# Performance work log

Measured on AMD Instinct MI355X. Metric: run time of the kernel, lower is better.

Reference implementation:

```python
import jax, jax.numpy as jnp
import numpy as np

B, N, D, H = 2, 2048, 1024, 16
DH = D // H  # 64


def setup_inputs() -> dict:
    key = jax.random.key(0)
    ks = jax.random.split(key, 5)
    s = 1.0 / np.sqrt(D)
    x = jax.random.normal(ks[0], (B, N, D), jnp.float32)
    # per-head kqv Linear weights, stacked: [H, D, 3*DH]
    Wkqv = jax.random.normal(ks[1], (H, D, 3 * DH), jnp.float32) * s
    bkqv = jax.random.normal(ks[2], (H, 3 * DH), jnp.float32) * 0.02
    Wo = jax.random.normal(ks[3], (D, D), jnp.float32) * s
    bo = jax.random.normal(ks[4], (D,), jnp.float32) * 0.02
    return {"x": x, "Wkqv": Wkqv, "bkqv": bkqv, "Wo": Wo, "bo": bo}


def reference(x, Wkqv, bkqv, Wo, bo):
    Bs, Ns, Ds = x.shape
    Hs = Wkqv.shape[0]
    dh = Wkqv.shape[-1] // 3
    # all heads' kqv projections at once: [B, H, N, 3*dh]
    kqv_out = jnp.einsum('bnd,hde->bhne', x, Wkqv) + bkqv[None, :, None, :]
    # original splits in order (k, q, v)
    k, q, v = jnp.split(kqv_out, 3, axis=-1)
    # NOTE: original computes attention_scores(k, q) = k @ q^T (swapped vs standard)
    A = jnp.einsum('bhnd,bhmd->bhnm', k, q) / jnp.sqrt(jnp.asarray(dh, x.dtype))
    mask = jnp.tril(jnp.ones((Ns, Ns), dtype=bool))
    A = jnp.where(mask[None, None], A, -jnp.inf)
    alpha = jax.nn.softmax(A, axis=-1)
    sa = jnp.einsum('bhnm,bhmd->bhnd', alpha, v)  # [B, H, N, dh]
    # concat heads along feature dim (head0..headH-1 order)
    sa = sa.transpose(0, 2, 1, 3).reshape(Bs, Ns, Hs * dh)
    return sa @ Wo + bo
```

## Files before the change

kernel.cpp:

```cpp
#include <hip/hip_runtime.h>
#include <hip/hip_bf16.h>
#include <cstdint>
#include <cstddef>

typedef __bf16 bf16x8 __attribute__((ext_vector_type(8)));
typedef __bf16 bf16x4 __attribute__((ext_vector_type(4)));
typedef float  f32x4  __attribute__((ext_vector_type(4)));

constexpr int Bc = 2, Nc = 2048, Dc = 1024, Hc = 16, DHc = 64;
constexpr int BN = Bc * Nc;
constexpr int E3 = 3 * DHc;
constexpr int BH = Bc * Hc;
constexpr int NK = Hc * E3;

__device__ __forceinline__ f32x4 mfma16(bf16x8 a, bf16x8 b, f32x4 c) {
  return __builtin_amdgcn_mfma_f32_16x16x32_bf16(a, b, c, 0, 0, 0);
}

__device__ __forceinline__ void gload16(const __bf16* g, __bf16* l) {
  __builtin_amdgcn_global_load_lds((const __attribute__((address_space(1))) void*)g,
                                   (__attribute__((address_space(3))) void*)l,
                                   16, 0, 0);
}

__global__ void cvt_x_kernel(const float* __restrict__ x, __bf16* __restrict__ xb) {
  int i = (blockIdx.x * 256 + threadIdx.x) * 4;
  float4 v = *(const float4*)(x + i);
  xb[i + 0] = (__bf16)v.x;
  xb[i + 1] = (__bf16)v.y;
  xb[i + 2] = (__bf16)v.z;
  xb[i + 3] = (__bf16)v.w;
}

constexpr int TP = 68;
__global__ void cvt_T_kernel(const float* __restrict__ src, __bf16* __restrict__ dst,
                             int R, int C) {
  __shared__ __bf16 T[64][TP];
  const int c0 = blockIdx.x * 64, r0 = blockIdx.y * 64;
  const size_t sbase = (size_t)blockIdx.z * R * C;
  const int tid = threadIdx.x;
#pragma unroll
  for (int it = 0; it < 4; ++it) {
    int g = tid + it * 256;
    int r = g >> 4, c4 = (g & 15) * 4;
    float4 v = *(const float4*)&src[sbase + (size_t)(r0 + r) * C + c0 + c4];
    T[c4 + 0][r] = (__bf16)v.x;
    T[c4 + 1][r] = (__bf16)v.y;
    T[c4 + 2][r] = (__bf16)v.z;
    T[c4 + 3][r] = (__bf16)v.w;
  }
  __syncthreads();
#pragma unroll
  for (int it = 0; it < 2; ++it) {
    int g = tid + it * 256;
    int c = g >> 3, ch = (g & 7) * 8;
    bf16x4 u0 = *(const bf16x4*)&T[c][ch];
    bf16x4 u1 = *(const bf16x4*)&T[c][ch + 4];
    __bf16* dp = &dst[sbase + (size_t)(c0 + c) * R + r0 + ch];
    *(bf16x4*)dp = u0;
    *(bf16x4*)(dp + 4) = u1;
  }
}

__launch_bounds__(256)
__global__ void kqv_gemm_kernel(const __bf16* __restrict__ xb,
                                const __bf16* __restrict__ wkt,
                                const float* __restrict__ bkqv,
                                __bf16* __restrict__ kqv,
                                __bf16* __restrict__ vT) {
  const int mt = blockIdx.x;
  const int nt = blockIdx.y;
  __shared__ __align__(16) __bf16 Al[2][128][64];
  __shared__ __align__(16) __bf16 Bl[2][128][64];
  const int tid  = threadIdx.x;
  const int lane = tid & 63;
  const int w    = tid >> 6;
  const int fr   = lane & 15, fq = lane >> 4;
  const int fq4  = fq * 4;
  const int WR   = (w >> 1) * 64, WC = (w & 1) * 64;
  const int sr   = tid >> 3;
  const int sc8  = ((tid & 7) ^ (sr & 7)) * 8;
  const int wb   = (w << 3);
  const int m0   = mt * 128, n0 = nt * 128;

  auto STAGE = [&](int buf, int k0) {
#pragma unroll
    for (int j = 0; j < 4; ++j)
      gload16(&xb[(size_t)(m0 + j * 32 + sr) * Dc + k0 + sc8], &Al[buf][j * 32 + wb][0]);
#pragma unroll
    for (int j = 0; j < 4; ++j)
      gload16(&wkt[(size_t)(n0 + j * 32 + sr) * Dc + k0 + sc8], &Bl[buf][j * 32 + wb][0]);
  };

  f32x4 acc[4][4] = {};
  STAGE(0, 0);
  int cur = 0;
  for (int t = 0; t < 16; ++t) {
    if (t < 15) {
      STAGE(cur ^ 1, (t + 1) * 64);
      asm volatile("s_waitcnt vmcnt(8)" ::: "memory");
    } else {
      asm volatile("s_waitcnt vmcnt(0)" ::: "memory");
    }
    asm volatile("s_barrier" ::: "memory");
    const char* Ab = (const char*)&Al[cur][0][0];
    const char* Bb = (const char*)&Bl[cur][0][0];
#pragma unroll
    for (int ks = 0; ks < 2; ++ks) {
      bf16x8 a_[4], b_[4];
#pragma unroll
      for (int mr = 0; mr < 4; ++mr) {
        int r = WR + mr * 16 + fr;
        a_[mr] = *(const bf16x8*)(Ab + r * 128 + ((ks * 64 + fq * 16) ^ ((r & 7) << 4)));
      }
#pragma unroll
      for (int nc = 0; nc < 4; ++nc) {
        int r = WC + nc * 16 + fr;
        b_[nc] = *(const bf16x8*)(Bb + r * 128 + ((ks * 64 + fq * 16) ^ ((r & 7) << 4)));
      }
#pragma unroll
      for (int mr = 0; mr < 4; ++mr)
#pragma unroll
        for (int nc = 0; nc < 4; ++nc)
          acc[mr][nc] = mfma16(a_[mr], b_[nc], acc[mr][nc]);
    }
    asm volatile("s_barrier" ::: "memory");
    cur ^= 1;
  }

  const int b = m0 >> 11;
#pragma unroll
  for (int nc = 0; nc < 4; ++nc) {
    const int nb = n0 + WC + nc * 16;
    const int h  = nb / 192;
    const int eb = nb - h * 192;
    const float bias = bkqv[nb + fr];
    if (eb < 64) {
      const float sc = 0.125f * 1.44269504088896f;
      const int el = eb + fr;
#pragma unroll
      for (int mr = 0; mr < 4; ++mr) {
        int nn0 = (m0 & (Nc - 1)) + WR + mr * 16 + fq4;
        bf16x4 v4;
#pragma unroll
        for (int i = 0; i < 4; ++i) v4[i] = (__bf16)((acc[mr][nc][i] + bias) * sc);
        *(bf16x4*)&kqv[((size_t)((b * Hc + h) * DHc + el)) * Nc + nn0] = v4;
      }
    } else if (eb < 128) {
      const int e = (eb - 64) + fr;
      __bf16* dst = kqv + (size_t)BH * Nc * DHc +
                    ((size_t)(b * Hc + h)) * Nc * DHc + e;
#pragma unroll
      for (int mr = 0; mr < 4; ++mr)
#pragma unroll
        for (int i = 0; i < 4; ++i) {
          int n = (m0 & (Nc - 1)) + WR + mr * 16 + fq4 + i;
          dst[(size_t)n * DHc] = (__bf16)(acc[mr][nc][i] + bias);
        }
    } else {
      const int el = eb - 128 + fr;
#pragma unroll
      for (int mr = 0; mr < 4; ++mr) {
        int nn0 = (m0 & (Nc - 1)) + WR + mr * 16 + fq4;
        bf16x4 v4;
#pragma unroll
        for (int i = 0; i < 4; ++i) v4[i] = (__bf16)(acc[mr][nc][i] + bias);
        *(bf16x4*)&vT[((size_t)((b * Hc + h) * DHc + el)) * Nc + nn0] = v4;
      }
    }
  }
}

__launch_bounds__(256)
__global__ void attn_kernel(const __bf16* __restrict__ kT,
                            const __bf16* __restrict__ qb,
                            const __bf16* __restrict__ vT,
                            __bf16* __restrict__ sab) {
  const int bx = blockIdx.x;
  const int by = blockIdx.y;
  const int bh   = 4 * (bx & 7) + (by >> 3);
  const int pair = (bx >> 3) * 8 + (by & 7);
  __shared__ __align__(16) __bf16 KqL[2][64][64];
  __shared__ __align__(16) __bf16 VtL[2][64][64];
  __shared__ __align__(16) __bf16 Pl[4][16][64];
  const int tid  = threadIdx.x;
  const int lane = tid & 63;
  const int w    = tid >> 6;
  const int fr   = lane & 15, fq = lane >> 4;
  const int fq4  = fq * 4;
  const int key  = (fr & 7) << 4;
  const int off0 = (fq * 16) ^ key;
  const int off1 = (fq * 16 + 64) ^ key;
  const __bf16* kth = kT + (size_t)bh * DHc * Nc;
  const __bf16* qbh = qb + (size_t)bh * Nc * DHc;
  const __bf16* vth = vT + (size_t)bh * DHc * Nc;
  const int b = bh >> 4, h = bh & 15;
  char* Pw = (char*)&Pl[w][0][0];

  const int sch  = (tid & 7);
  const int r_s0 = tid >> 3;
  const int r_s1 = r_s0 + 32;
  const int swb0 = r_s0 * 128 + ((sch * 16) ^ ((r_s0 & 7) << 4));
  const int swb1 = r_s1 * 128 + ((sch * 16) ^ ((r_s1 & 7) << 4));

  for (int ph = 0; ph < 2; ++ph) {
    const int qt   = ph ? (31 - pair) : pair;
    const int n0   = qt * 64 + w * 16;
    const int ncol = n0 + fr;

    bf16x8 bq0, bq1;
#pragma unroll
    for (int j = 0; j < 8; ++j) {
      bq0[j] = kth[(size_t)(8 * fq + j) * Nc + n0 + fr];
      bq1[j] = kth[(size_t)(32 + 8 * fq + j) * Nc + n0 + fr];
    }

    float l_run = 0.f;
    f32x4 acc[4] = {};

    __syncthreads();
    {
      bf16x8 k0a = *(const bf16x8*)&qbh[(size_t)r_s0 * DHc + sch * 8];
      bf16x8 k0b = *(const bf16x8*)&qbh[(size_t)r_s1 * DHc + sch * 8];
      bf16x8 v0a = *(const bf16x8*)&vth[(size_t)r_s0 * Nc + sch * 8];
      bf16x8 v0b = *(const bf16x8*)&vth[(size_t)r_s1 * Nc + sch * 8];
      *(bf16x8*)((char*)&KqL[0][0][0] + swb0) = k0a;
      *(bf16x8*)((char*)&KqL[0][0][0] + swb1) = k0b;
      *(bf16x8*)((char*)&VtL[0][0][0] + swb0) = v0a;
      *(bf16x8*)((char*)&VtL[0][0][0] + swb1) = v0b;
    }
    __syncthreads();

    int cur = 0;
    for (int t = 0; t <= qt; ++t) {
      bf16x8 nk0, nk1, nv0, nv1;
      const bool more = (t < qt);
      if (more) {
        const int v1 = (t + 1) * 64;
        nk0 = *(const bf16x8*)&qbh[(size_t)(v1 + r_s0) * DHc + sch * 8];
        nk1 = *(const bf16x8*)&qbh[(size_t)(v1 + r_s1) * DHc + sch * 8];
        nv0 = *(const bf16x8*)&vth[(size_t)r_s0 * Nc + v1 + sch * 8];
        nv1 = *(const bf16x8*)&vth[(size_t)r_s1 * Nc + v1 + sch * 8];
      }

      const char* Kqb = (const char*)&KqL[cur][0][0];
      const char* Vtb = (const char*)&VtL[cur][0][0];

      f32x4 s[4];
      __builtin_amdgcn_s_setprio(1);
#pragma unroll
      for (int c = 0; c < 4; ++c) {
        const char* rp = Kqb + (c * 16 + fr) * 128;
        bf16x8 t0 = *(const bf16x8*)(rp + off0);
        bf16x8 t1 = *(const bf16x8*)(rp + off1);
        f32x4 z = {};
        z = mfma16(t0, bq0, z);
        z = mfma16(t1, bq1, z);
        s[c] = z;
      }
      __builtin_amdgcn_s_setprio(0);

      if (t == qt) {
        const int thr = ncol - t * 64;
#pragma unroll
        for (int c = 0; c < 4; ++c)
#pragma unroll
          for (int i = 0; i < 4; ++i) {
            float pv = exp2f(s[c][i]);
            s[c][i] = (c * 16 + fq4 + i > thr) ? 0.f : pv;
          }
      } else {
#pragma unroll
        for (int c = 0; c < 4; ++c)
#pragma unroll
          for (int i = 0; i < 4; ++i) s[c][i] = exp2f(s[c][i]);
      }
      float cs0 = (s[0][0] + s[0][1]) + (s[0][2] + s[0][3]);
      float cs1 = (s[1][0] + s[1][1]) + (s[1][2] + s[1][3]);
      float cs2 = (s[2][0] + s[2][1]) + (s[2][2] + s[2][3]);
      float cs3 = (s[3][0] + s[3][1]) + (s[3][2] + s[3][3]);
      l_run += (cs0 + cs1) + (cs2 + cs3);

#pragma unroll
      for (int c = 0; c < 4; ++c) {
        bf16x4 p4;
#pragma unroll
        for (int i = 0; i < 4; ++i) p4[i] = (__bf16)s[c][i];
        *(bf16x4*)(Pw + fr * 128 + ((c * 32 + fq * 8) ^ key)) = p4;
      }
      asm volatile("s_waitcnt lgkmcnt(0)" ::: "memory");
      __builtin_amdgcn_sched_barrier(0);

      __builtin_amdgcn_s_setprio(1);
      bf16x8 ap0 = *(const bf16x8*)(Pw + fr * 128 + off0);
      bf16x8 ap1 = *(const bf16x8*)(Pw + fr * 128 + off1);
#pragma unroll
      for (int d = 0; d < 4; ++d) {
        const char* vp = Vtb + (d * 16 + fr) * 128;
        bf16x8 bv0 = *(const bf16x8*)(vp + off0);
        bf16x8 bv1 = *(const bf16x8*)(vp + off1);
        acc[d] = mfma16(ap0, bv0, acc[d]);
        acc[d] = mfma16(ap1, bv1, acc[d]);
      }
      __builtin_amdgcn_s_setprio(0);

      if (more) {
        char* Kn = (char*)&KqL[cur ^ 1][0][0];
        char* Vn = (char*)&VtL[cur ^ 1][0][0];
        *(bf16x8*)(Kn + swb0) = nk0;
        *(bf16x8*)(Kn + swb1) = nk1;
        *(bf16x8*)(Vn + swb0) = nv0;
        *(bf16x8*)(Vn + swb1) = nv1;
      }
      __syncthreads();
      cur ^= 1;
    }

    l_run += __shfl_xor(l_run, 16);
    l_run += __shfl_xor(l_run, 32);
    float linv[4];
#pragma unroll
    for (int ii = 0; ii < 4; ++ii) linv[ii] = 1.0f / __shfl(l_run, fq4 + ii);
#pragma unroll
    for (int d = 0; d < 4; ++d)
#pragma unroll
      for (int ii = 0; ii < 4; ++ii) {
        int n  = n0 + fq4 + ii;
        int dd = d * 16 + fr;
        sab[((size_t)(b * Nc + n)) * Dc + h * DHc + dd] = (__bf16)(acc[d][ii] * linv[ii]);
      }
  }
}

__launch_bounds__(256)
__global__ void out_gemm_kernel(const __bf16* __restrict__ sab,
                                const __bf16* __restrict__ wot,
                                const float* __restrict__ bo,
                                float* __restrict__ out) {
  const int mt = blockIdx.x;
  const int nt = blockIdx.y;
  __shared__ __align__(16) __bf16 Al[2][128][64];
  __shared__ __align__(16) __bf16 Bl[2][128][64];
  const int tid  = threadIdx.x;
  const int lane = tid & 63;
  const int w    = tid >> 6;
  const int fr   = lane & 15, fq = lane >> 4;
  const int fq4  = fq * 4;
  const int WR   = (w >> 1) * 64, WC = (w & 1) * 64;
  const int sr   = tid >> 3;
  const int sc8  = ((tid & 7) ^ (sr & 7)) * 8;
  const int wb   = (w << 3);
  const int m0   = mt * 128, n0 = nt * 128;

  auto STAGE = [&](int buf, int k0) {
#pragma unroll
    for (int j = 0; j < 4; ++j)
      gload16(&sab[(size_t)(m0 + j * 32 + sr) * Dc + k0 + sc8], &Al[buf][j * 32 + wb][0]);
#pragma unroll
    for (int j = 0; j < 4; ++j)
      gload16(&wot[(size_t)(n0 + j * 32 + sr) * Dc + k0 + sc8], &Bl[buf][j * 32 + wb][0]);
  };

  f32x4 acc[4][4] = {};
  STAGE(0, 0);
  int cur = 0;
  for (int t = 0; t < 16; ++t) {
    if (t < 15) {
      STAGE(cur ^ 1, (t + 1) * 64);
      asm volatile("s_waitcnt vmcnt(8)" ::: "memory");
    } else {
      asm volatile("s_waitcnt vmcnt(0)" ::: "memory");
    }
    asm volatile("s_barrier" ::: "memory");
    const char* Ab = (const char*)&Al[cur][0][0];
    const char* Bb = (const char*)&Bl[cur][0][0];
#pragma unroll
    for (int ks = 0; ks < 2; ++ks) {
      bf16x8 a_[4], b_[4];
#pragma unroll
      for (int mr = 0; mr < 4; ++mr) {
        int r = WR + mr * 16 + fr;
        a_[mr] = *(const bf16x8*)(Ab + r * 128 + ((ks * 64 + fq * 16) ^ ((r & 7) << 4)));
      }
#pragma unroll
      for (int nc = 0; nc < 4; ++nc) {
        int r = WC + nc * 16 + fr;
        b_[nc] = *(const bf16x8*)(Bb + r * 128 + ((ks * 64 + fq * 16) ^ ((r & 7) << 4)));
      }
#pragma unroll
      for (int mr = 0; mr < 4; ++mr)
#pragma unroll
        for (int nc = 0; nc < 4; ++nc)
          acc[mr][nc] = mfma16(a_[mr], b_[nc], acc[mr][nc]);
    }
    asm volatile("s_barrier" ::: "memory");
    cur ^= 1;
  }
#pragma unroll
  for (int mr = 0; mr < 4; ++mr)
#pragma unroll
    for (int nc = 0; nc < 4; ++nc)
#pragma unroll
      for (int i = 0; i < 4; ++i) {
        int m = m0 + WR + mr * 16 + fq4 + i;
        int e = n0 + WC + nc * 16 + fr;
        out[(size_t)m * Dc + e] = acc[mr][nc][i] + bo[e];
      }
}

extern "C" void kernel_launch(void* const* d_in, const int* in_sizes, int n_in,
                              void* d_out, int out_size, void* d_ws, size_t ws_size,
                              hipStream_t stream) {
  const float* x    = (const float*)d_in[0];
  const float* Wkqv = (const float*)d_in[1];
  const float* bkqv = (const float*)d_in[2];
  const float* Wo   = (const float*)d_in[3];
  const float* bo   = (const float*)d_in[4];
  float* out = (float*)d_out;

  __bf16* xb   = (__bf16*)d_ws;
  __bf16* wkt  = xb  + (size_t)BN * Dc;
  __bf16* wot  = wkt + (size_t)NK * Dc;
  __bf16* kqv  = wot + (size_t)Dc * Dc;
  __bf16* kTb  = kqv;
  __bf16* qbuf = kqv + (size_t)BH * Nc * DHc;
  __bf16* vTb  = kqv + 2 * (size_t)BH * Nc * DHc;
  __bf16* sab  = kqv + 3 * (size_t)BH * Nc * DHc;

  cvt_x_kernel<<<(BN * Dc) / (256 * 4), 256, 0, stream>>>(x, xb);
  cvt_T_kernel<<<dim3(E3 / 64, Dc / 64, Hc), 256, 0, stream>>>(Wkqv, wkt, Dc, E3);
  cvt_T_kernel<<<dim3(Dc / 64, Dc / 64, 1), 256, 0, stream>>>(Wo, wot, Dc, Dc);

  kqv_gemm_kernel<<<dim3(BN / 128, NK / 128), 256, 0, stream>>>(xb, wkt, bkqv, kqv, vTb);

  attn_kernel<<<dim3(16, BH), 256, 0, stream>>>(kTb, qbuf, vTb, sab);

  out_gemm_kernel<<<dim3(BN / 128, Dc / 128), 256, 0, stream>>>(sab, wot, bo, out);
}
```

Measured before the change: 117.9 us.

## Split causal attention key range into two halves and combine partials

Each query tile's key loop is split into two halves run by separate blocks, which doubles the grid from 512 to 1024 blocks. Each block writes its unnormalized partial output (bf16) and row sums to scratch reused from the x and weight conversion buffers. A new combine kernel adds the two partials and normalizes them. The aim is more parallelism and occupancy on the attention stage, paid for with an extra kernel launch, extra memory traffic for the partials, and bf16 rounding of the unnormalized partial sums.

```diff
diff --git a/kernel.cpp b/kernel.cpp
--- a/kernel.cpp
+++ b/kernel.cpp
@@ -175,11 +175,16 @@
 __global__ void attn_kernel(const __bf16* __restrict__ kT,
                             const __bf16* __restrict__ qb,
                             const __bf16* __restrict__ vT,
-                            __bf16* __restrict__ sab) {
+                            __bf16* __restrict__ pA,
+                            __bf16* __restrict__ pB,
+                            float* __restrict__ lA,
+                            float* __restrict__ lB) {
   const int bx = blockIdx.x;
   const int by = blockIdx.y;
   const int bh   = 4 * (bx & 7) + (by >> 3);
-  const int pair = (bx >> 3) * 8 + (by & 7);
+  const int u    = (bx >> 3) | ((by & 7) << 2);
+  const int pair = u & 15;
+  const int hf   = u >> 4;
   __shared__ __align__(16) __bf16 KqL[2][64][64];
   __shared__ __align__(16) __bf16 VtL[2][64][64];
   __shared__ __align__(16) __bf16 Pl[4][16][64];
@@ -196,6 +201,8 @@
   const __bf16* vth = vT + (size_t)bh * DHc * Nc;
   const int b = bh >> 4, h = bh & 15;
   char* Pw = (char*)&Pl[w][0][0];
+  __bf16* part = hf ? pB : pA;
+  float*  lprt = hf ? lB : lA;
 
   const int sch  = (tid & 7);
   const int r_s0 = tid >> 3;
@@ -205,131 +212,154 @@
 
   for (int ph = 0; ph < 2; ++ph) {
     const int qt   = ph ? (31 - pair) : pair;
+    const int mid  = (qt + 2) >> 1;
+    const int t0   = hf ? mid : 0;
+    const int t1   = hf ? (qt + 1) : mid;
     const int n0   = qt * 64 + w * 16;
     const int ncol = n0 + fr;
 
-    bf16x8 bq0, bq1;
-#pragma unroll
-    for (int j = 0; j < 8; ++j) {
-      bq0[j] = kth[(size_t)(8 * fq + j) * Nc + n0 + fr];
-      bq1[j] = kth[(size_t)(32 + 8 * fq + j) * Nc + n0 + fr];
-    }
-
     float l_run = 0.f;
     f32x4 acc[4] = {};
 
-    __syncthreads();
-    {
-      bf16x8 k0a = *(const bf16x8*)&qbh[(size_t)r_s0 * DHc + sch * 8];
-      bf16x8 k0b = *(const bf16x8*)&qbh[(size_t)r_s1 * DHc + sch * 8];
-      bf16x8 v0a = *(const bf16x8*)&vth[(size_t)r_s0 * Nc + sch * 8];
-      bf16x8 v0b = *(const bf16x8*)&vth[(size_t)r_s1 * Nc + sch * 8];
-      *(bf16x8*)((char*)&KqL[0][0][0] + swb0) = k0a;
-      *(bf16x8*)((char*)&KqL[0][0][0] + swb1) = k0b;
-      *(bf16x8*)((char*)&VtL[0][0][0] + swb0) = v0a;
-      *(bf16x8*)((char*)&VtL[0][0][0] + swb1) = v0b;
-    }
-    __syncthreads();
-
-    int cur = 0;
-    for (int t = 0; t <= qt; ++t) {
-      bf16x8 nk0, nk1, nv0, nv1;
-      const bool more = (t < qt);
-      if (more) {
-        const int v1 = (t + 1) * 64;
-        nk0 = *(const bf16x8*)&qbh[(size_t)(v1 + r_s0) * DHc + sch * 8];
-        nk1 = *(const bf16x8*)&qbh[(size_t)(v1 + r_s1) * DHc + sch * 8];
-        nv0 = *(const bf16x8*)&vth[(size_t)r_s0 * Nc + v1 + sch * 8];
-        nv1 = *(const bf16x8*)&vth[(size_t)r_s1 * Nc + v1 + sch * 8];
-      }
-
-      const char* Kqb = (const char*)&KqL[cur][0][0];
-      const char* Vtb = (const char*)&VtL[cur][0][0];
-
-      f32x4 s[4];
-      __builtin_amdgcn_s_setprio(1);
-#pragma unroll
-      for (int c = 0; c < 4; ++c) {
-        const char* rp = Kqb + (c * 16 + fr) * 128;
-        bf16x8 t0 = *(const bf16x8*)(rp + off0);
-        bf16x8 t1 = *(const bf16x8*)(rp + off1);
-        f32x4 z = {};
-        z = mfma16(t0, bq0, z);
-        z = mfma16(t1, bq1, z);
-        s[c] = z;
-      }
-      __builtin_amdgcn_s_setprio(0);
-
-      if (t == qt) {
-        const int thr = ncol - t * 64;
-#pragma unroll
-        for (int c = 0; c < 4; ++c)
-#pragma unroll
-          for (int i = 0; i < 4; ++i) {
-            float pv = exp2f(s[c][i]);
-            s[c][i] = (c * 16 + fq4 + i > thr) ? 0.f : pv;
-          }
-      } else {
-#pragma unroll
-        for (int c = 0; c < 4; ++c)
-#pragma unroll
-          for (int i = 0; i < 4; ++i) s[c][i] = exp2f(s[c][i]);
-      }
-      float cs0 = (s[0][0] + s[0][1]) + (s[0][2] + s[0][3]);
-      float cs1 = (s[1][0] + s[1][1]) + (s[1][2] + s[1][3]);
-      float cs2 = (s[2][0] + s[2][1]) + (s[2][2] + s[2][3]);
-      float cs3 = (s[3][0] + s[3][1]) + (s[3][2] + s[3][3]);
-      l_run += (cs0 + cs1) + (cs2 + cs3);
-
-#pragma unroll
-      for (int c = 0; c < 4; ++c) {
-        bf16x4 p4;
-#pragma unroll
-        for (int i = 0; i < 4; ++i) p4[i] = (__bf16)s[c][i];
-        *(bf16x4*)(Pw + fr * 128 + ((c * 32 + fq * 8) ^ key)) = p4;
-      }
-      asm volatile("s_waitcnt lgkmcnt(0)" ::: "memory");
-      __builtin_amdgcn_sched_barrier(0);
-
-      __builtin_amdgcn_s_setprio(1);
-      bf16x8 ap0 = *(const bf16x8*)(Pw + fr * 128 + off0);
-      bf16x8 ap1 = *(const bf16x8*)(Pw + fr * 128 + off1);
-#pragma unroll
-      for (int d = 0; d < 4; ++d) {
-        const char* vp = Vtb + (d * 16 + fr) * 128;
-        bf16x8 bv0 = *(const bf16x8*)(vp + off0);
-        bf16x8 bv1 = *(const bf16x8*)(vp + off1);
-        acc[d] = mfma16(ap0, bv0, acc[d]);
-        acc[d] = mfma16(ap1, bv1, acc[d]);
-      }
-      __builtin_amdgcn_s_setprio(0);
-
-      if (more) {
-        char* Kn = (char*)&KqL[cur ^ 1][0][0];
-        char* Vn = (char*)&VtL[cur ^ 1][0][0];
-        *(bf16x8*)(Kn + swb0) = nk0;
-        *(bf16x8*)(Kn + swb1) = nk1;
-        *(bf16x8*)(Vn + swb0) = nv0;
-        *(bf16x8*)(Vn + swb1) = nv1;
-      }
+    if (t0 < t1) {
+      bf16x8 bq0, bq1;
+#pragma unroll
+      for (int j = 0; j < 8; ++j) {
+        bq0[j] = kth[(size_t)(8 * fq + j) * Nc + n0 + fr];
+        bq1[j] = kth[(size_t)(32 + 8 * fq + j) * Nc + n0 + fr];
+      }
+
       __syncthreads();
-      cur ^= 1;
+      {
+        const int v0 = t0 * 64;
+        bf16x8 k0a = *(const bf16x8*)&qbh[(size_t)(v0 + r_s0) * DHc + sch * 8];
+        bf16x8 k0b = *(const bf16x8*)&qbh[(size_t)(v0 + r_s1) * DHc + sch * 8];
+        bf16x8 v0a = *(const bf16x8*)&vth[(size_t)r_s0 * Nc + v0 + sch * 8];
+        bf16x8 v0b = *(const bf16x8*)&vth[(size_t)r_s1 * Nc + v0 + sch * 8];
+        *(bf16x8*)((char*)&KqL[0][0][0] + swb0) = k0a;
+        *(bf16x8*)((char*)&KqL[0][0][0] + swb1) = k0b;
+        *(bf16x8*)((char*)&VtL[0][0][0] + swb0) = v0a;
+        *(bf16x8*)((char*)&VtL[0][0][0] + swb1) = v0b;
+      }
+      __syncthreads();
+
+      int cur = 0;
+      for (int t = t0; t < t1; ++t) {
+        bf16x8 nk0, nk1, nv0, nv1;
+        const bool more = (t + 1 < t1);
+        if (more) {
+          const int v1 = (t + 1) * 64;
+          nk0 = *(const bf16x8*)&qbh[(size_t)(v1 + r_s0) * DHc + sch * 8];
+          nk1 = *(const bf16x8*)&qbh[(size_t)(v1 + r_s1) * DHc + sch * 8];
+          nv0 = *(const bf16x8*)&vth[(size_t)r_s0 * Nc + v1 + sch * 8];
+          nv1 = *(const bf16x8*)&vth[(size_t)r_s1 * Nc + v1 + sch * 8];
+        }
+
+        const char* Kqb = (const char*)&KqL[cur][0][0];
+        const char* Vtb = (const char*)&VtL[cur][0][0];
+
+        f32x4 s[4];
+        __builtin_amdgcn_s_setprio(1);
+#pragma unroll
+        for (int c = 0; c < 4; ++c) {
+          const char* rp = Kqb + (c * 16 + fr) * 128;
+          bf16x8 t0v = *(const bf16x8*)(rp + off0);
+          bf16x8 t1v = *(const bf16x8*)(rp + off1);
+          f32x4 z = {};
+          z = mfma16(t0v, bq0, z);
+          z = mfma16(t1v, bq1, z);
+          s[c] = z;
+        }
+        __builtin_amdgcn_s_setprio(0);
+
+        if (t == qt) {
+          const int thr = ncol - t * 64;
+#pragma unroll
+          for (int c = 0; c < 4; ++c)
+#pragma unroll
+            for (int i = 0; i < 4; ++i) {
+              float pv = exp2f(s[c][i]);
+              s[c][i] = (c * 16 + fq4 + i > thr) ? 0.f : pv;
+            }
+        } else {
+#pragma unroll
+          for (int c = 0; c < 4; ++c)
+#pragma unroll
+            for (int i = 0; i < 4; ++i) s[c][i] = exp2f(s[c][i]);
+        }
+        float cs0 = (s[0][0] + s[0][1]) + (s[0][2] + s[0][3]);
+        float cs1 = (s[1][0] + s[1][1]) + (s[1][2] + s[1][3]);
+        float cs2 = (s[2][0] + s[2][1]) + (s[2][2] + s[2][3]);
+        float cs3 = (s[3][0] + s[3][1]) + (s[3][2] + s[3][3]);
+        l_run += (cs0 + cs1) + (cs2 + cs3);
+
+#pragma unroll
+        for (int c = 0; c < 4; ++c) {
+          bf16x4 p4;
+#pragma unroll
+          for (int i = 0; i < 4; ++i) p4[i] = (__bf16)s[c][i];
+          *(bf16x4*)(Pw + fr * 128 + ((c * 32 + fq * 8) ^ key)) = p4;
+        }
+        asm volatile("s_waitcnt lgkmcnt(0)" ::: "memory");
+        __builtin_amdgcn_sched_barrier(0);
+
+        __builtin_amdgcn_s_setprio(1);
+        bf16x8 ap0 = *(const bf16x8*)(Pw + fr * 128 + off0);
+        bf16x8 ap1 = *(const bf16x8*)(Pw + fr * 128 + off1);
+#pragma unroll
+        for (int d = 0; d < 4; ++d) {
+          const char* vp = Vtb + (d * 16 + fr) * 128;
+          bf16x8 bv0 = *(const bf16x8*)(vp + off0);
+          bf16x8 bv1 = *(const bf16x8*)(vp + off1);
+          acc[d] = mfma16(ap0, bv0, acc[d]);
+          acc[d] = mfma16(ap1, bv1, acc[d]);
+        }
+        __builtin_amdgcn_s_setprio(0);
+
+        if (more) {
+          char* Kn = (char*)&KqL[cur ^ 1][0][0];
+          char* Vn = (char*)&VtL[cur ^ 1][0][0];
+          *(bf16x8*)(Kn + swb0) = nk0;
+          *(bf16x8*)(Kn + swb1) = nk1;
+          *(bf16x8*)(Vn + swb0) = nv0;
+          *(bf16x8*)(Vn + swb1) = nv1;
+        }
+        __syncthreads();
+        cur ^= 1;
+      }
     }
 
     l_run += __shfl_xor(l_run, 16);
     l_run += __shfl_xor(l_run, 32);
-    float linv[4];
-#pragma unroll
-    for (int ii = 0; ii < 4; ++ii) linv[ii] = 1.0f / __shfl(l_run, fq4 + ii);
+    if (fq == 0) lprt[(size_t)bh * Nc + n0 + fr] = l_run;
 #pragma unroll
     for (int d = 0; d < 4; ++d)
 #pragma unroll
       for (int ii = 0; ii < 4; ++ii) {
         int n  = n0 + fq4 + ii;
         int dd = d * 16 + fr;
-        sab[((size_t)(b * Nc + n)) * Dc + h * DHc + dd] = (__bf16)(acc[d][ii] * linv[ii]);
-      }
-  }
+        part[((size_t)(b * Nc + n)) * Dc + h * DHc + dd] = (__bf16)acc[d][ii];
+      }
+  }
+}
+
+__global__ void combine_kernel(const __bf16* __restrict__ pA,
+                               __bf16* __restrict__ sab,
+                               const float* __restrict__ lA,
+                               const float* __restrict__ lB) {
+  const int idx = (blockIdx.x * 256 + threadIdx.x) * 8;
+  const int m = idx >> 10;
+  const int e = idx & 1023;
+  const int h = e >> 6;
+  const int b = m >> 11, n = m & (Nc - 1);
+  const size_t li = (size_t)(b * Hc + h) * Nc + n;
+  const float linv = 1.0f / (lA[li] + lB[li]);
+  bf16x8 a = *(const bf16x8*)(pA + idx);
+  bf16x8 c = *(const bf16x8*)(sab + idx);
+  bf16x8 o;
+#pragma unroll
+  for (int j = 0; j < 8; ++j) o[j] = (__bf16)(((float)a[j] + (float)c[j]) * linv);
+  *(bf16x8*)(sab + idx) = o;
 }
 
 __launch_bounds__(256)
@@ -427,13 +457,19 @@
   __bf16* vTb  = kqv + 2 * (size_t)BH * Nc * DHc;
   __bf16* sab  = kqv + 3 * (size_t)BH * Nc * DHc;
 
+  __bf16* pA = xb;
+  float*  lA = (float*)wkt;
+  float*  lB = lA + (size_t)BH * Nc;
+
   cvt_x_kernel<<<(BN * Dc) / (256 * 4), 256, 0, stream>>>(x, xb);
   cvt_T_kernel<<<dim3(E3 / 64, Dc / 64, Hc), 256, 0, stream>>>(Wkqv, wkt, Dc, E3);
   cvt_T_kernel<<<dim3(Dc / 64, Dc / 64, 1), 256, 0, stream>>>(Wo, wot, Dc, Dc);
 
   kqv_gemm_kernel<<<dim3(BN / 128, NK / 128), 256, 0, stream>>>(xb, wkt, bkqv, kqv, vTb);
 
-  attn_kernel<<<dim3(16, BH), 256, 0, stream>>>(kTb, qbuf, vTb, sab);
+  attn_kernel<<<dim3(32, 32), 256, 0, stream>>>(kTb, qbuf, vTb, pA, sab, lA, lB);
+
+  combine_kernel<<<(BN * Dc) / (256 * 8), 256, 0, stream>>>(pA, sab, lA, lB);
 
   out_gemm_kernel<<<dim3(BN / 128, Dc / 128), 256, 0, stream>>>(sab, wot, bo, out);
 }
```

New measurement: 122.9 us. +4.3%, slower.

## Process both paired query tiles in one merged KV sweep sharing loads

Applied to the files above, without the earlier changes.

Each attention block used to handle two causal query tiles (pair and 31-pair) one after the other, streaming the shared KV prefix twice. The two tiles are now processed together in one loop over the longer tile's KV range, so each K/V LDS tile and fragment is loaded once and used for both tiles while the shorter tile is active. This halves KV global and LDS traffic for the overlapping prefix and removes the per-phase startup cost, at the price of doubled accumulator and score registers and a second P buffer in LDS, which may lower occupancy.

```diff
diff --git a/kernel.cpp b/kernel.cpp
--- a/kernel.cpp
+++ b/kernel.cpp
@@ -182,7 +182,7 @@
   const int pair = (bx >> 3) * 8 + (by & 7);
   __shared__ __align__(16) __bf16 KqL[2][64][64];
   __shared__ __align__(16) __bf16 VtL[2][64][64];
-  __shared__ __align__(16) __bf16 Pl[4][16][64];
+  __shared__ __align__(16) __bf16 Pl[4][2][16][64];
   const int tid  = threadIdx.x;
   const int lane = tid & 63;
   const int w    = tid >> 6;
@@ -195,7 +195,8 @@
   const __bf16* qbh = qb + (size_t)bh * Nc * DHc;
   const __bf16* vth = vT + (size_t)bh * DHc * Nc;
   const int b = bh >> 4, h = bh & 15;
-  char* Pw = (char*)&Pl[w][0][0];
+  char* PwA = (char*)&Pl[w][0][0][0];
+  char* PwB = (char*)&Pl[w][1][0][0];
 
   const int sch  = (tid & 7);
   const int r_s0 = tid >> 3;
@@ -203,133 +204,190 @@
   const int swb0 = r_s0 * 128 + ((sch * 16) ^ ((r_s0 & 7) << 4));
   const int swb1 = r_s1 * 128 + ((sch * 16) ^ ((r_s1 & 7) << 4));
 
-  for (int ph = 0; ph < 2; ++ph) {
-    const int qt   = ph ? (31 - pair) : pair;
-    const int n0   = qt * 64 + w * 16;
-    const int ncol = n0 + fr;
-
-    bf16x8 bq0, bq1;
-#pragma unroll
-    for (int j = 0; j < 8; ++j) {
-      bq0[j] = kth[(size_t)(8 * fq + j) * Nc + n0 + fr];
-      bq1[j] = kth[(size_t)(32 + 8 * fq + j) * Nc + n0 + fr];
-    }
-
-    float l_run = 0.f;
-    f32x4 acc[4] = {};
-
-    __syncthreads();
-    {
-      bf16x8 k0a = *(const bf16x8*)&qbh[(size_t)r_s0 * DHc + sch * 8];
-      bf16x8 k0b = *(const bf16x8*)&qbh[(size_t)r_s1 * DHc + sch * 8];
-      bf16x8 v0a = *(const bf16x8*)&vth[(size_t)r_s0 * Nc + sch * 8];
-      bf16x8 v0b = *(const bf16x8*)&vth[(size_t)r_s1 * Nc + sch * 8];
-      *(bf16x8*)((char*)&KqL[0][0][0] + swb0) = k0a;
-      *(bf16x8*)((char*)&KqL[0][0][0] + swb1) = k0b;
-      *(bf16x8*)((char*)&VtL[0][0][0] + swb0) = v0a;
-      *(bf16x8*)((char*)&VtL[0][0][0] + swb1) = v0b;
-    }
-    __syncthreads();
-
-    int cur = 0;
-    for (int t = 0; t <= qt; ++t) {
-      bf16x8 nk0, nk1, nv0, nv1;
-      const bool more = (t < qt);
-      if (more) {
-        const int v1 = (t + 1) * 64;
-        nk0 = *(const bf16x8*)&qbh[(size_t)(v1 + r_s0) * DHc + sch * 8];
-        nk1 = *(const bf16x8*)&qbh[(size_t)(v1 + r_s1) * DHc + sch * 8];
-        nv0 = *(const bf16x8*)&vth[(size_t)r_s0 * Nc + v1 + sch * 8];
-        nv1 = *(const bf16x8*)&vth[(size_t)r_s1 * Nc + v1 + sch * 8];
-      }
-
-      const char* Kqb = (const char*)&KqL[cur][0][0];
-      const char* Vtb = (const char*)&VtL[cur][0][0];
-
-      f32x4 s[4];
-      __builtin_amdgcn_s_setprio(1);
-#pragma unroll
-      for (int c = 0; c < 4; ++c) {
-        const char* rp = Kqb + (c * 16 + fr) * 128;
-        bf16x8 t0 = *(const bf16x8*)(rp + off0);
-        bf16x8 t1 = *(const bf16x8*)(rp + off1);
-        f32x4 z = {};
-        z = mfma16(t0, bq0, z);
-        z = mfma16(t1, bq1, z);
-        s[c] = z;
-      }
-      __builtin_amdgcn_s_setprio(0);
-
-      if (t == qt) {
-        const int thr = ncol - t * 64;
+  const int qtA = pair, qtB = 31 - pair;
+  const int n0A = qtA * 64 + w * 16, n0B = qtB * 64 + w * 16;
+  const int ncolA = n0A + fr, ncolB = n0B + fr;
+
+  bf16x8 bqA0, bqA1, bqB0, bqB1;
+#pragma unroll
+  for (int j = 0; j < 8; ++j) {
+    bqA0[j] = kth[(size_t)(8 * fq + j) * Nc + n0A + fr];
+    bqA1[j] = kth[(size_t)(32 + 8 * fq + j) * Nc + n0A + fr];
+    bqB0[j] = kth[(size_t)(8 * fq + j) * Nc + n0B + fr];
+    bqB1[j] = kth[(size_t)(32 + 8 * fq + j) * Nc + n0B + fr];
+  }
+
+  float lA = 0.f, lB = 0.f;
+  f32x4 accA[4] = {}, accB[4] = {};
+
+  {
+    bf16x8 k0a = *(const bf16x8*)&qbh[(size_t)r_s0 * DHc + sch * 8];
+    bf16x8 k0b = *(const bf16x8*)&qbh[(size_t)r_s1 * DHc + sch * 8];
+    bf16x8 v0a = *(const bf16x8*)&vth[(size_t)r_s0 * Nc + sch * 8];
+    bf16x8 v0b = *(const bf16x8*)&vth[(size_t)r_s1 * Nc + sch * 8];
+    *(bf16x8*)((char*)&KqL[0][0][0] + swb0) = k0a;
+    *(bf16x8*)((char*)&KqL[0][0][0] + swb1) = k0b;
+    *(bf16x8*)((char*)&VtL[0][0][0] + swb0) = v0a;
+    *(bf16x8*)((char*)&VtL[0][0][0] + swb1) = v0b;
+  }
+  __syncthreads();
+
+  int cur = 0;
+  for (int t = 0; t <= qtB; ++t) {
+    bf16x8 nk0, nk1, nv0, nv1;
+    const bool more = (t < qtB);
+    if (more) {
+      const int v1 = (t + 1) * 64;
+      nk0 = *(const bf16x8*)&qbh[(size_t)(v1 + r_s0) * DHc + sch * 8];
+      nk1 = *(const bf16x8*)&qbh[(size_t)(v1 + r_s1) * DHc + sch * 8];
+      nv0 = *(const bf16x8*)&vth[(size_t)r_s0 * Nc + v1 + sch * 8];
+      nv1 = *(const bf16x8*)&vth[(size_t)r_s1 * Nc + v1 + sch * 8];
+    }
+    const bool doA = (t <= qtA);
+
+    const char* Kqb = (const char*)&KqL[cur][0][0];
+    const char* Vtb = (const char*)&VtL[cur][0][0];
+
+    f32x4 sB[4], sA[4];
+    __builtin_amdgcn_s_setprio(1);
+#pragma unroll
+    for (int c = 0; c < 4; ++c) {
+      const char* rp = Kqb + (c * 16 + fr) * 128;
+      bf16x8 t0 = *(const bf16x8*)(rp + off0);
+      bf16x8 t1 = *(const bf16x8*)(rp + off1);
+      f32x4 z = {};
+      z = mfma16(t0, bqB0, z);
+      z = mfma16(t1, bqB1, z);
+      sB[c] = z;
+      if (doA) {
+        f32x4 y = {};
+        y = mfma16(t0, bqA0, y);
+        y = mfma16(t1, bqA1, y);
+        sA[c] = y;
+      }
+    }
+    __builtin_amdgcn_s_setprio(0);
+
+    if (t == qtB) {
+      const int thr = ncolB - t * 64;
+#pragma unroll
+      for (int c = 0; c < 4; ++c)
+#pragma unroll
+        for (int i = 0; i < 4; ++i) {
+          float pv = exp2f(sB[c][i]);
+          sB[c][i] = (c * 16 + fq4 + i > thr) ? 0.f : pv;
+        }
+    } else {
+#pragma unroll
+      for (int c = 0; c < 4; ++c)
+#pragma unroll
+        for (int i = 0; i < 4; ++i) sB[c][i] = exp2f(sB[c][i]);
+    }
+    lB += ((sB[0][0] + sB[0][1]) + (sB[0][2] + sB[0][3])) +
+          ((sB[1][0] + sB[1][1]) + (sB[1][2] + sB[1][3])) +
+          ((sB[2][0] + sB[2][1]) + (sB[2][2] + sB[2][3])) +
+          ((sB[3][0] + sB[3][1]) + (sB[3][2] + sB[3][3]));
+    if (doA) {
+      if (t == qtA) {
+        const int thr = ncolA - t * 64;
 #pragma unroll
         for (int c = 0; c < 4; ++c)
 #pragma unroll
           for (int i = 0; i < 4; ++i) {
-            float pv = exp2f(s[c][i]);
-            s[c][i] = (c * 16 + fq4 + i > thr) ? 0.f : pv;
+            float pv = exp2f(sA[c][i]);
+            sA[c][i] = (c * 16 + fq4 + i > thr) ? 0.f : pv;
           }
       } else {
 #pragma unroll
         for (int c = 0; c < 4; ++c)
 #pragma unroll
-          for (int i = 0; i < 4; ++i) s[c][i] = exp2f(s[c][i]);
-      }
-      float cs0 = (s[0][0] + s[0][1]) + (s[0][2] + s[0][3]);
-      float cs1 = (s[1][0] + s[1][1]) + (s[1][2] + s[1][3]);
-      float cs2 = (s[2][0] + s[2][1]) + (s[2][2] + s[2][3]);
-      float cs3 = (s[3][0] + s[3][1]) + (s[3][2] + s[3][3]);
-      l_run += (cs0 + cs1) + (cs2 + cs3);
-
+          for (int i = 0; i < 4; ++i) sA[c][i] = exp2f(sA[c][i]);
+      }
+      lA += ((sA[0][0] + sA[0][1]) + (sA[0][2] + sA[0][3])) +
+            ((sA[1][0] + sA[1][1]) + (sA[1][2] + sA[1][3])) +
+            ((sA[2][0] + sA[2][1]) + (sA[2][2] + sA[2][3])) +
+            ((sA[3][0] + sA[3][1]) + (sA[3][2] + sA[3][3]));
+    }
+
+#pragma unroll
+    for (int c = 0; c < 4; ++c) {
+      bf16x4 p4;
+#pragma unroll
+      for (int i = 0; i < 4; ++i) p4[i] = (__bf16)sB[c][i];
+      *(bf16x4*)(PwB + fr * 128 + ((c * 32 + fq * 8) ^ key)) = p4;
+    }
+    if (doA) {
 #pragma unroll
       for (int c = 0; c < 4; ++c) {
         bf16x4 p4;
 #pragma unroll
-        for (int i = 0; i < 4; ++i) p4[i] = (__bf16)s[c][i];
-        *(bf16x4*)(Pw + fr * 128 + ((c * 32 + fq * 8) ^ key)) = p4;
-      }
-      asm volatile("s_waitcnt lgkmcnt(0)" ::: "memory");
-      __builtin_amdgcn_sched_barrier(0);
-
-      __builtin_amdgcn_s_setprio(1);
-      bf16x8 ap0 = *(const bf16x8*)(Pw + fr * 128 + off0);
-      bf16x8 ap1 = *(const bf16x8*)(Pw + fr * 128 + off1);
+        for (int i = 0; i < 4; ++i) p4[i] = (__bf16)sA[c][i];
+        *(bf16x4*)(PwA + fr * 128 + ((c * 32 + fq * 8) ^ key)) = p4;
+      }
+    }
+    asm volatile("s_waitcnt lgkmcnt(0)" ::: "memory");
+    __builtin_amdgcn_sched_barrier(0);
+
+    __builtin_amdgcn_s_setprio(1);
+    bf16x8 apB0 = *(const bf16x8*)(PwB + fr * 128 + off0);
+    bf16x8 apB1 = *(const bf16x8*)(PwB + fr * 128 + off1);
+    if (doA) {
+      bf16x8 apA0 = *(const bf16x8*)(PwA + fr * 128 + off0);
+      bf16x8 apA1 = *(const bf16x8*)(PwA + fr * 128 + off1);
 #pragma unroll
       for (int d = 0; d < 4; ++d) {
         const char* vp = Vtb + (d * 16 + fr) * 128;
         bf16x8 bv0 = *(const bf16x8*)(vp + off0);
         bf16x8 bv1 = *(const bf16x8*)(vp + off1);
-        acc[d] = mfma16(ap0, bv0, acc[d]);
-        acc[d] = mfma16(ap1, bv1, acc[d]);
-      }
-      __builtin_amdgcn_s_setprio(0);
-
-      if (more) {
-        char* Kn = (char*)&KqL[cur ^ 1][0][0];
-        char* Vn = (char*)&VtL[cur ^ 1][0][0];
-        *(bf16x8*)(Kn + swb0) = nk0;
-        *(bf16x8*)(Kn + swb1) = nk1;
-        *(bf16x8*)(Vn + swb0) = nv0;
-        *(bf16x8*)(Vn + swb1) = nv1;
-      }
-      __syncthreads();
-      cur ^= 1;
-    }
-
-    l_run += __shfl_xor(l_run, 16);
-    l_run += __shfl_xor(l_run, 32);
-    float linv[4];
-#pragma unroll
-    for (int ii = 0; ii < 4; ++ii) linv[ii] = 1.0f / __shfl(l_run, fq4 + ii);
-#pragma unroll
-    for (int d = 0; d < 4; ++d)
-#pragma unroll
-      for (int ii = 0; ii < 4; ++ii) {
-        int n  = n0 + fq4 + ii;
-        int dd = d * 16 + fr;
-        sab[((size_t)(b * Nc + n)) * Dc + h * DHc + dd] = (__bf16)(acc[d][ii] * linv[ii]);
-      }
-  }
+        accB[d] = mfma16(apB0, bv0, accB[d]);
+        accB[d] = mfma16(apB1, bv1, accB[d]);
+        accA[d] = mfma16(apA0, bv0, accA[d]);
+        accA[d] = mfma16(apA1, bv1, accA[d]);
+      }
+    } else {
+#pragma unroll
+      for (int d = 0; d < 4; ++d) {
+        const char* vp = Vtb + (d * 16 + fr) * 128;
+        bf16x8 bv0 = *(const bf16x8*)(vp + off0);
+        bf16x8 bv1 = *(const bf16x8*)(vp + off1);
+        accB[d] = mfma16(apB0, bv0, accB[d]);
+        accB[d] = mfma16(apB1, bv1, accB[d]);
+      }
+    }
+    __builtin_amdgcn_s_setprio(0);
+
+    if (more) {
+      char* Kn = (char*)&KqL[cur ^ 1][0][0];
+      char* Vn = (char*)&VtL[cur ^ 1][0][0];
+      *(bf16x8*)(Kn + swb0) = nk0;
+      *(bf16x8*)(Kn + swb1) = nk1;
+      *(bf16x8*)(Vn + swb0) = nv0;
+      *(bf16x8*)(Vn + swb1) = nv1;
+    }
+    __syncthreads();
+    cur ^= 1;
+  }
+
+  lA += __shfl_xor(lA, 16);
+  lA += __shfl_xor(lA, 32);
+  lB += __shfl_xor(lB, 16);
+  lB += __shfl_xor(lB, 32);
+  float liA[4], liB[4];
+#pragma unroll
+  for (int ii = 0; ii < 4; ++ii) {
+    liA[ii] = 1.0f / __shfl(lA, fq4 + ii);
+    liB[ii] = 1.0f / __shfl(lB, fq4 + ii);
+  }
+#pragma unroll
+  for (int d = 0; d < 4; ++d)
+#pragma unroll
+    for (int ii = 0; ii < 4; ++ii) {
+      int dd = d * 16 + fr;
+      sab[((size_t)(b * Nc + n0A + fq4 + ii)) * Dc + h * DHc + dd] =
+          (__bf16)(accA[d][ii] * liA[ii]);
+      sab[((size_t)(b * Nc + n0B + fq4 + ii)) * Dc + h * DHc + dd] =
+          (__bf16)(accB[d][ii] * liB[ii]);
+    }
 }
 
 __launch_bounds__(256)
```

Result: slower. 124.8 us (+5.8%).
